# Kernel tuning notes

Hardware: AMD Instinct MI355X
Metric: run time of the kernel (lower is better)

Reference implementation:

```python
import jax, jax.numpy as jnp
import numpy as np

B, NC, NF, D = 4, 256, 768, 768
TOK_RATIO = 0.5
LN_EPS = 1e-5


def _linear(x, w, b):
    # w: [D_in, D_out]
    return x @ w + b


def _leaky(x):
    return jax.nn.leaky_relu(x, negative_slope=0.01)


def setup_inputs() -> dict:
    key = jax.random.key(0)
    ks = jax.random.split(key, 12)
    s = 1.0 / np.sqrt(D)
    inp = {
        "cls_tokens": jax.random.normal(ks[0], (B, NC, D), dtype=jnp.float32),
        "feats": jax.random.normal(ks[1], (B, NF, D), dtype=jnp.float32),
        "W_head_w": jax.random.uniform(ks[2], (D, D), minval=-s, maxval=s),
        "W_head_b": jax.random.uniform(ks[3], (D,), minval=-s, maxval=s),
        "W_tail_w": jax.random.uniform(ks[4], (D, D), minval=-s, maxval=s),
        "W_tail_b": jax.random.uniform(ks[5], (D,), minval=-s, maxval=s),
        "lin1_w": jax.random.uniform(ks[6], (D, D), minval=-s, maxval=s),
        "lin1_b": jax.random.uniform(ks[7], (D,), minval=-s, maxval=s),
        "lin2_w": jax.random.uniform(ks[8], (D, D), minval=-s, maxval=s),
        "lin2_b": jax.random.uniform(ks[9], (D,), minval=-s, maxval=s),
        "ln_w": jnp.ones((D,), dtype=jnp.float32),
        "ln_b": jnp.zeros((D,), dtype=jnp.float32),
    }
    return inp


def reference(cls_tokens, feats, W_head_w, W_head_b, W_tail_w, W_tail_b,
              lin1_w, lin1_b, lin2_w, lin2_b, ln_w, ln_b):
    topk = int(TOK_RATIO * NC)
    scale = D ** (-0.5)

    # feats is detached in the original (clone().detach())
    x = jnp.concatenate([cls_tokens, jax.lax.stop_gradient(feats)], axis=1)  # [B, Nt, D]

    e_h = _linear(cls_tokens, W_head_w, W_head_b)  # [B, Nc, D]
    e_t = _linear(x, W_tail_w, W_tail_b)           # [B, Nt, D]

    attn_logit = jnp.einsum('bnd,bmd->bnm', e_h * scale, e_t)  # [B, Nc, Nt]
    topk_weight, topk_index = jax.lax.top_k(attn_logit, topk)  # [B, Nc, k]

    # Gather neighbor embeddings: Nb_h[b, n, j] = e_t[b, topk_index[b, n, j]]
    Nb_h = jax.vmap(lambda et, idx: et[idx])(e_t, topk_index)  # [B, Nc, k, D]

    topk_prob = jax.nn.softmax(topk_weight, axis=2)            # [B, Nc, k]
    p = topk_prob[..., None]
    eh_r = p * Nb_h + (1.0 - p) * e_h[:, :, None, :]           # [B, Nc, k, D]

    gate = jnp.tanh(e_h[:, :, None, :] + eh_r)
    ka_weight = jnp.einsum('bnkd,bnkd->bnk', Nb_h, gate)
    ka_prob = jax.nn.softmax(ka_weight, axis=2)
    e_Nh = jnp.einsum('bnk,bnkd->bnd', ka_prob, Nb_h)          # [B, Nc, D]

    # bi-interaction aggregation
    sum_emb = _leaky(_linear((e_h + e_Nh) * 0.1 + cls_tokens, lin1_w, lin1_b))
    bi_emb = _leaky(_linear(e_h * e_Nh * 0.1 + cls_tokens, lin2_w, lin2_b))
    embedding = sum_emb + bi_emb

    # LayerNorm (dropout is a no-op: p=0 and output overwritten in original)
    mu = jnp.mean(embedding, axis=-1, keepdims=True)
    var = jnp.var(embedding, axis=-1, keepdims=True)
    h = (embedding - mu) * jax.lax.rsqrt(var + LN_EPS) * ln_w + ln_b
    return h
```

## Files before the change

### kernel.cpp

```cpp
#include <hip/hip_runtime.h>
#include <hip/hip_bf16.h>
#include <math.h>

#define DDIM 768
#define NCLS 256
#define NFEAT 768
#define NTOK 1024
#define NBATCH 4
#define KSEL 128

typedef float f32x4 __attribute__((ext_vector_type(4)));
typedef float f32x2 __attribute__((ext_vector_type(2)));
typedef short s16x8 __attribute__((ext_vector_type(8)));

#if __has_builtin(__builtin_amdgcn_exp2f)
#define EXP2F __builtin_amdgcn_exp2f
#else
#define EXP2F(x) __expf(0.6931471805599453f * (x))
#endif

__device__ __forceinline__ float wsum(float v) {
#pragma unroll
  for (int o = 32; o; o >>= 1) v += __shfl_down(v, o, 64);
  return v;
}
__device__ __forceinline__ float wmaxr(float v) {
#pragma unroll
  for (int o = 32; o; o >>= 1) v = fmaxf(v, __shfl_down(v, o, 64));
  return v;
}
__device__ __forceinline__ short f2bf(float f) {
  union { __hip_bfloat16 h; short s; } u;
  u.h = __float2bfloat16(f);
  return u.s;
}
__device__ __forceinline__ float bf2f(short s) {
  union { unsigned u; float f; } c;
  c.u = ((unsigned)(unsigned short)s) << 16;
  return c.f;
}
__device__ __forceinline__ f32x2 bfpair(unsigned w) {
  f32x2 r;
  r.x = __uint_as_float(w << 16);
  r.y = __uint_as_float(w & 0xffff0000u);
  return r;
}
__device__ __forceinline__ void cvt8(float4 x, float4 y, s16x8& h, s16x8& l) {
  float v[8] = {x.x, x.y, x.z, x.w, y.x, y.y, y.z, y.w};
#pragma unroll
  for (int i = 0; i < 8; ++i) {
    short hh = f2bf(v[i]);
    h[i] = hh;
    l[i] = f2bf(v[i] - bf2f(hh));
  }
}
__device__ __forceinline__ int swz(int row, int chunk) {
  return (row << 5) + (((chunk ^ (row >> 1)) & 3) << 3);
}

__global__ __launch_bounds__(256) void prep_all(
    const float* __restrict__ cls, const float* __restrict__ feats,
    const float* __restrict__ w0, const float* __restrict__ w1,
    const float* __restrict__ w2, const float* __restrict__ w3,
    short* __restrict__ h0, short* __restrict__ h1, short* __restrict__ h2,
    short* __restrict__ h3, short* __restrict__ l0, short* __restrict__ l1,
    short* __restrict__ Xh, short* __restrict__ Xl) {
  __shared__ float tile[32][33];
  const int bid = blockIdx.x;
  const int t = threadIdx.x;
  if (bid < 2304) {
    const int z = bid / 576, rem = bid % 576;
    const int by = rem / 24, bx = rem % 24;
    const float* s = z == 0 ? w0 : z == 1 ? w1 : z == 2 ? w2 : w3;
    short* dh = z == 0 ? h0 : z == 1 ? h1 : z == 2 ? h2 : h3;
    short* dl = z == 0 ? l0 : z == 1 ? l1 : nullptr;
    const int tx = t & 31, ty0 = t >> 5;
    const int r0 = by * 32, c0 = bx * 32;
#pragma unroll
    for (int i = 0; i < 4; ++i) {
      int ty = ty0 + i * 8;
      tile[ty][tx] = s[(size_t)(r0 + ty) * DDIM + c0 + tx];
    }
    __syncthreads();
#pragma unroll
    for (int i = 0; i < 4; ++i) {
      int ty = ty0 + i * 8;
      float v = tile[tx][ty];
      short hh = f2bf(v);
      dh[(size_t)(c0 + ty) * DDIM + r0 + tx] = hh;
      if (dl) dl[(size_t)(c0 + ty) * DDIM + r0 + tx] = f2bf(v - bf2f(hh));
    }
  } else {
    const size_t base = ((size_t)(bid - 2304) * 256 + t) * 8;
    const int row = (int)(base / DDIM);
    const int col = (int)(base % DDIM);
    const int b = row >> 10, rr = row & 1023;
    const float* src =
        (rr < NCLS) ? cls + ((size_t)b * NCLS + rr) * DDIM + col
                    : feats + ((size_t)b * NFEAT + (rr - NCLS)) * DDIM + col;
    float4 a0 = *(const float4*)(src);
    float4 a1 = *(const float4*)(src + 4);
    s16x8 h, l;
    cvt8(a0, a1, h, l);
    *(s16x8*)(Xh + base) = h;
    *(s16x8*)(Xl + base) = l;
  }
}

__global__ __launch_bounds__(256) void gemm_front(
    const short* __restrict__ Xh, const short* __restrict__ Xl,
    const short* __restrict__ WhT_h, const short* __restrict__ WhT_l,
    const float* __restrict__ Whb, const short* __restrict__ WtT_h,
    const short* __restrict__ WtT_l, const float* __restrict__ Wtb,
    short* __restrict__ eh_hi, short* __restrict__ eh_lo,
    short* __restrict__ et_hi, short* __restrict__ et_lo) {
  __shared__ short Ah[128 * 32], Al[128 * 32];
  __shared__ short Bh[64 * 32], Bl[64 * 32];
  const int bid = blockIdx.x;
  const int xcd = bid & 7, idx = bid >> 3;
  const int ytile = xcd * 5 + idx / 12;
  const int xtile = idx % 12;
  const int t = threadIdx.x;
  const int row0 = ytile * 128, col0 = xtile * 64;
  const bool head = row0 < 1024;

  const int ar = t >> 1, ac = (t & 1) * 2;
  const int aw0 = swz(ar, ac), aw1 = swz(ar, ac + 1);
  size_t xrow;
  {
    int gr = row0 + ar;
    xrow = head ? (size_t)(((gr >> 8) << 10) + (gr & 255)) : (size_t)(gr - 1024);
  }
  const short* aph = Xh + xrow * DDIM + ac * 8;
  const short* apl = Xl + xrow * DDIM + ac * 8;
  const int br = t >> 2, bc = t & 3;
  const int bw0 = swz(br, bc);
  const short* bph = (head ? WhT_h : WtT_h) + (size_t)(col0 + br) * DDIM + bc * 8;
  const short* bpl = (head ? WhT_l : WtT_l) + (size_t)(col0 + br) * DDIM + bc * 8;
  const float* biasu = head ? Whb : Wtb;

  const int lane = t & 63, wave = t >> 6;
  const int wr = wave >> 1, wc = wave & 1;
  const int fr = lane & 15, fq = lane >> 4;

  f32x4 acc[4][2] = {};
  s16x8 rah0 = *(const s16x8*)(aph);
  s16x8 rah1 = *(const s16x8*)(aph + 8);
  s16x8 ral0 = *(const s16x8*)(apl);
  s16x8 ral1 = *(const s16x8*)(apl + 8);
  s16x8 rbh = *(const s16x8*)(bph);
  s16x8 rbl = *(const s16x8*)(bpl);

  for (int kt = 0; kt < 24; ++kt) {
    __syncthreads();
    *(s16x8*)&Ah[aw0] = rah0;
    *(s16x8*)&Ah[aw1] = rah1;
    *(s16x8*)&Al[aw0] = ral0;
    *(s16x8*)&Al[aw1] = ral1;
    *(s16x8*)&Bh[bw0] = rbh;
    *(s16x8*)&Bl[bw0] = rbl;
    __syncthreads();
    const int kn = (kt < 23 ? kt + 1 : 23) * 32;
    rah0 = *(const s16x8*)(aph + kn);
    rah1 = *(const s16x8*)(aph + kn + 8);
    ral0 = *(const s16x8*)(apl + kn);
    ral1 = *(const s16x8*)(apl + kn + 8);
    rbh = *(const s16x8*)(bph + kn);
    rbl = *(const s16x8*)(bpl + kn);

    s16x8 afh[4], afl[4];
#pragma unroll
    for (int m = 0; m < 4; ++m) {
      int ao = swz(wr * 64 + m * 16 + fr, fq);
      afh[m] = *(const s16x8*)&Ah[ao];
      afl[m] = *(const s16x8*)&Al[ao];
    }
#pragma unroll
    for (int n = 0; n < 2; ++n) {
      int bo = swz(wc * 32 + n * 16 + fr, fq);
      s16x8 bfh = *(const s16x8*)&Bh[bo];
      s16x8 bfl = *(const s16x8*)&Bl[bo];
#pragma unroll
      for (int m = 0; m < 4; ++m) {
        acc[m][n] =
            __builtin_amdgcn_mfma_f32_16x16x32_bf16(afh[m], bfh, acc[m][n], 0, 0, 0);
        acc[m][n] =
            __builtin_amdgcn_mfma_f32_16x16x32_bf16(afh[m], bfl, acc[m][n], 0, 0, 0);
        acc[m][n] =
            __builtin_amdgcn_mfma_f32_16x16x32_bf16(afl[m], bfh, acc[m][n], 0, 0, 0);
      }
    }
  }

  short* Ch = head ? eh_hi : et_hi;
  short* Cl = head ? eh_lo : et_lo;
  const int rbase = head ? row0 : row0 - 1024;
#pragma unroll
  for (int m = 0; m < 4; ++m) {
#pragma unroll
    for (int n = 0; n < 2; ++n) {
#pragma unroll
      for (int r = 0; r < 4; ++r) {
        int rg = rbase + wr * 64 + m * 16 + fq * 4 + r;
        int cg = col0 + wc * 32 + n * 16 + fr;
        float v = acc[m][n][r] + biasu[cg];
        size_t o = (size_t)rg * DDIM + cg;
        short hh = f2bf(v);
        Ch[o] = hh;
        Cl[o] = f2bf(v - bf2f(hh));
      }
    }
  }
}

__global__ __launch_bounds__(256) void gemm_logits(
    const short* __restrict__ eh_hi, const short* __restrict__ eh_lo,
    const short* __restrict__ et_hi, const short* __restrict__ et_lo,
    float* __restrict__ logits, float scale) {
  __shared__ short Ah[32 * 32], Al[32 * 32];
  __shared__ short Bh[64 * 32], Bl[64 * 32];
  const int bid = blockIdx.x;
  const int xcd = bid & 7, idx = bid >> 3;
  const int batch = xcd >> 1;
  const int sub = ((xcd & 1) << 6) | idx;
  const int xtile = sub & 15, ytile = sub >> 4;
  const int row0 = ytile * 32, col0 = xtile * 64;
  const int t = threadIdx.x;

  const int ahalf = t >> 7, ac2 = t & 127;
  const int asr = ac2 >> 2, acc_ = ac2 & 3;
  const short* aptr = (ahalf ? eh_lo : eh_hi) +
                      ((size_t)batch * NCLS + row0 + asr) * DDIM + acc_ * 8;
  const int aso = swz(asr, acc_);
  const int bsr = t >> 2, bcc = t & 3;
  const short* bph = et_hi + ((size_t)batch * NTOK + col0 + bsr) * DDIM + bcc * 8;
  const short* bpl = et_lo + ((size_t)batch * NTOK + col0 + bsr) * DDIM + bcc * 8;
  const int bso = swz(bsr, bcc);

  const int lane = t & 63, wave = t >> 6;
  const int wr = wave >> 1, wc = wave & 1;
  const int fr = lane & 15, fq = lane >> 4;

  f32x4 acc[2] = {};
  s16x8 rA = *(const s16x8*)(aptr);
  s16x8 rbh = *(const s16x8*)(bph);
  s16x8 rbl = *(const s16x8*)(bpl);

  for (int kt = 0; kt < 24; ++kt) {
    __syncthreads();
    *(s16x8*)&(ahalf ? Al : Ah)[aso] = rA;
    *(s16x8*)&Bh[bso] = rbh;
    *(s16x8*)&Bl[bso] = rbl;
    __syncthreads();
    const int kn = (kt < 23 ? kt + 1 : 23) * 32;
    rA = *(const s16x8*)(aptr + kn);
    rbh = *(const s16x8*)(bph + kn);
    rbl = *(const s16x8*)(bpl + kn);
    int ao = swz(wr * 16 + fr, fq);
    s16x8 afh = *(const s16x8*)&Ah[ao];
    s16x8 afl = *(const s16x8*)&Al[ao];
#pragma unroll
    for (int n = 0; n < 2; ++n) {
      int bo = swz(wc * 32 + n * 16 + fr, fq);
      s16x8 bfh = *(const s16x8*)&Bh[bo];
      s16x8 bfl = *(const s16x8*)&Bl[bo];
      acc[n] = __builtin_amdgcn_mfma_f32_16x16x32_bf16(afh, bfh, acc[n], 0, 0, 0);
      acc[n] = __builtin_amdgcn_mfma_f32_16x16x32_bf16(afh, bfl, acc[n], 0, 0, 0);
      acc[n] = __builtin_amdgcn_mfma_f32_16x16x32_bf16(afl, bfh, acc[n], 0, 0, 0);
    }
  }

  float* Cb = logits + (size_t)batch * NCLS * NTOK;
#pragma unroll
  for (int n = 0; n < 2; ++n)
#pragma unroll
    for (int r = 0; r < 4; ++r) {
      int rg = row0 + wr * 16 + fq * 4 + r;
      int cg = col0 + wc * 32 + n * 16 + fr;
      Cb[(size_t)rg * NTOK + cg] = scale * acc[n][r];
    }
}

__global__ __launch_bounds__(512) void select_agg(
    const float* __restrict__ logits, const short* __restrict__ eh_hi,
    const short* __restrict__ et_hi, const float* __restrict__ cls,
    short* __restrict__ inbf) {
  const int bid = blockIdx.x;
  const int xcd = bid & 7, slot = bid >> 3;
  const int batch = xcd >> 1;
  const int row = batch * 256 + (xcd & 1) * 128 + slot;
  const int t = threadIdx.x, lane = t & 63, wave = t >> 6;

  __shared__ int hist[256];
  __shared__ int sh_bin, sh_rem;
  __shared__ int cnt;
  __shared__ int wsumT[8];
  __shared__ float p_sh[KSEL];
  __shared__ int idx_sh[KSEL];
  __shared__ float kaw_sh[KSEL];
  __shared__ float red[2];

  float2 v2 = *(const float2*)(logits + (size_t)row * NTOK + 2 * t);
  float val[2] = {v2.x, v2.y};
  unsigned key[2];
#pragma unroll
  for (int i = 0; i < 2; ++i) {
    unsigned u = __float_as_uint(val[i]);
    key[i] = (u & 0x80000000u) ? ~u : (u | 0x80000000u);
  }
  unsigned pref = 0, mask = 0;
  int rem = KSEL;
#pragma unroll
  for (int shift = 24; shift >= 0; shift -= 8) {
    if (t < 256) hist[t] = 0;
    __syncthreads();
#pragma unroll
    for (int i = 0; i < 2; ++i)
      if ((key[i] & mask) == pref)
        atomicAdd(&hist[(key[i] >> shift) & 255], 1);
    __syncthreads();
    if (wave == 0) {
      int h0 = hist[4 * lane], h1 = hist[4 * lane + 1];
      int h2 = hist[4 * lane + 2], h3 = hist[4 * lane + 3];
      int s = h0 + h1 + h2 + h3;
#pragma unroll
      for (int o = 1; o < 64; o <<= 1) {
        int v = __shfl_down(s, o, 64);
        if (lane + o < 64) s += v;
      }
      int abv = __shfl_down(s, 1, 64);
      if (lane == 63) abv = 0;
      int c3 = abv + h3, c2 = c3 + h2, c1 = c2 + h1, c0 = c1 + h0;
      int bin = -1, nab = 0;
      if (c3 >= rem && abv < rem) { bin = 4 * lane + 3; nab = abv; }
      else if (c2 >= rem && c3 < rem) { bin = 4 * lane + 2; nab = c3; }
      else if (c1 >= rem && c2 < rem) { bin = 4 * lane + 1; nab = c2; }
      else if (c0 >= rem && c1 < rem) { bin = 4 * lane + 0; nab = c1; }
      if (bin >= 0) { sh_bin = bin; sh_rem = rem - nab; }
    }
    __syncthreads();
    pref |= ((unsigned)sh_bin) << shift;
    mask |= 0xFFu << shift;
    rem = sh_rem;
  }
  const unsigned T = pref;
  const int above = KSEL - rem;

  if (t == 0) cnt = 0;
  int tc = (key[0] == T) + (key[1] == T);
  int inc = tc;
#pragma unroll
  for (int o = 1; o < 64; o <<= 1) {
    int v = __shfl_up(inc, o, 64);
    if (lane >= o) inc += v;
  }
  if (lane == 63) wsumT[wave] = inc;
  __syncthreads();
  int wbase = 0;
#pragma unroll
  for (int w = 0; w < 8; ++w)
    if (w < wave) wbase += wsumT[w];
  int excl = wbase + inc - tc;
#pragma unroll
  for (int i = 0; i < 2; ++i) {
    if (key[i] > T) {
      int s2 = atomicAdd(&cnt, 1);
      p_sh[s2] = val[i];
      idx_sh[s2] = 2 * t + i;
    } else if (key[i] == T) {
      int r = excl++;
      if (r < rem) {
        p_sh[above + r] = val[i];
        idx_sh[above + r] = 2 * t + i;
      }
    }
  }
  __syncthreads();

  if (wave == 0) {
    float m = wmaxr(fmaxf(p_sh[lane], p_sh[lane + 64]));
    if (!lane) red[0] = m;
  }
  __syncthreads();
  if (t < KSEL) p_sh[t] = __expf(p_sh[t] - red[0]);
  __syncthreads();
  if (wave == 0) {
    float s = wsum(p_sh[lane] + p_sh[lane + 64]);
    if (!lane) red[1] = s;
  }
  __syncthreads();
  if (t < KSEL) p_sh[t] *= (1.f / red[1]);
  __syncthreads();

  f32x2 eh2[6];
  {
    const short* ehrow = eh_hi + (size_t)row * DDIM;
    s16x8 e8 = *(const s16x8*)(ehrow + 8 * lane);
    short4 e4 = *(const short4*)(ehrow + 512 + 4 * lane);
    const unsigned* w8 = (const unsigned*)&e8;
    const unsigned* w4 = (const unsigned*)&e4;
#pragma unroll
    for (int i = 0; i < 4; ++i) eh2[i] = bfpair(w8[i]);
    eh2[4] = bfpair(w4[0]);
    eh2[5] = bfpair(w4[1]);
  }
  const short* etb = et_hi + (size_t)batch * NTOK * DDIM;
  const float LOG2E = 1.4426950408889634f;

  {
    const int jb = wave * 16;
    const short* nb0 = etb + (size_t)idx_sh[jb] * DDIM;
    s16x8 n8 = *(const s16x8*)(nb0 + 8 * lane);
    short4 n4 = *(const short4*)(nb0 + 512 + 4 * lane);
    for (int i = 0; i < 16; ++i) {
      const int j = jb + i;
      s16x8 n8n;
      short4 n4n;
      if (i < 15) {
        const short* nbn = etb + (size_t)idx_sh[j + 1] * DDIM;
        n8n = *(const s16x8*)(nbn + 8 * lane);
        n4n = *(const short4*)(nbn + 512 + 4 * lane);
      }
      float pj = p_sh[j];
      float a2 = (4.f - 2.f * pj) * LOG2E;
      float b22 = (2.f * pj) * LOG2E;
      f32x2 av = {a2, a2}, bv = {b22, b22};
      f32x2 acc2 = {0.f, 0.f};
      const unsigned* w8 = (const unsigned*)&n8;
      const unsigned* w4 = (const unsigned*)&n4;
      f32x2 nq2[6];
#pragma unroll
      for (int q = 0; q < 4; ++q) nq2[q] = bfpair(w8[q]);
      nq2[4] = bfpair(w4[0]);
      nq2[5] = bfpair(w4[1]);
#pragma unroll
      for (int q = 0; q < 6; ++q) {
        f32x2 arg = av * eh2[q] + bv * nq2[q];
        f32x2 ex;
        ex.x = EXP2F(arg.x);
        ex.y = EXP2F(arg.y);
        f32x2 den = ex + (f32x2){1.f, 1.f};
        f32x2 r;
        r.x = __builtin_amdgcn_rcpf(den.x);
        r.y = __builtin_amdgcn_rcpf(den.y);
        f32x2 g = r * (f32x2){-2.f, -2.f} + (f32x2){1.f, 1.f};
        acc2 = nq2[q] * g + acc2;
      }
      float partial = acc2.x + acc2.y;
      partial = wsum(partial);
      if (!lane) kaw_sh[j] = partial;
      n8 = n8n;
      n4 = n4n;
    }
  }
  __syncthreads();

  if (wave == 0) {
    float m = wmaxr(fmaxf(kaw_sh[lane], kaw_sh[lane + 64]));
    if (!lane) red[0] = m;
  }
  __syncthreads();
  if (t < KSEL) kaw_sh[t] = __expf(kaw_sh[t] - red[0]);
  __syncthreads();
  if (wave == 0) {
    float s = wsum(kaw_sh[lane] + kaw_sh[lane + 64]);
    if (!lane) red[1] = s;
  }
  __syncthreads();
  if (t < KSEL) kaw_sh[t] *= (1.f / red[1]);
  __syncthreads();

  if (t < 384) {
    const size_t o = (size_t)row * DDIM + 2 * t;
    unsigned ehw = *(const unsigned*)(eh_hi + o);
    f32x2 eh = bfpair(ehw);
    float2 cl2 = *(const float2*)(cls + o);
    f32x2 cl = {cl2.x, cl2.y};
    f32x2 acc = {0.f, 0.f};
#pragma unroll 8
    for (int j = 0; j < KSEL; ++j) {
      float pr = kaw_sh[j];
      unsigned w = *(const unsigned*)(etb + (size_t)idx_sh[j] * DDIM + 2 * t);
      f32x2 nb = bfpair(w);
      acc = nb * (f32x2){pr, pr} + acc;
    }
    f32x2 sv = (eh + acc) * (f32x2){0.1f, 0.1f} + cl;
    f32x2 bvv = (eh * acc) * (f32x2){0.1f, 0.1f} + cl;
    short2 s2, b2;
    s2.x = f2bf(sv.x);
    s2.y = f2bf(sv.y);
    b2.x = f2bf(bvv.x);
    b2.y = f2bf(bvv.y);
    *(short2*)&inbf[o] = s2;
    *(short2*)&inbf[(size_t)(NBATCH * NCLS) * DDIM + o] = b2;
  }
}

__global__ __launch_bounds__(256) void gemm_lin(
    const short* __restrict__ inbf, const short* __restrict__ L1T,
    const short* __restrict__ L2T, const float* __restrict__ b1,
    const float* __restrict__ b2, float* __restrict__ emb) {
  __shared__ short A1[32 * 32], A2[32 * 32];
  __shared__ short B1[64 * 32], B2[64 * 32];
  const int bid = blockIdx.x;
  const int xcd = bid & 7, idx = bid >> 3;
  const int ytile = xcd * 4 + idx / 12, xtile = idx % 12;
  const int t = threadIdx.x;
  const int row0 = ytile * 32, col0 = xtile * 64;

  const int ahalf = t >> 7, at = t & 127;
  const int asr = at >> 2, asc = at & 3;
  const short* aptr = inbf + (ahalf ? (size_t)1024 * DDIM : 0) +
                      (size_t)(row0 + asr) * DDIM + asc * 8;
  const int aso = swz(asr, asc);
  const int bsr = t >> 2, bsc = t & 3;
  const short* b1p = L1T + (size_t)(col0 + bsr) * DDIM + bsc * 8;
  const short* b2p = L2T + (size_t)(col0 + bsr) * DDIM + bsc * 8;
  const int bso = swz(bsr, bsc);

  const int lane = t & 63, wave = t >> 6;
  const int wr = wave >> 1, wc = wave & 1;
  const int fr = lane & 15, fq = lane >> 4;

  f32x4 acc1[2] = {}, acc2[2] = {};
  s16x8 rA = *(const s16x8*)(aptr);
  s16x8 rB1 = *(const s16x8*)(b1p);
  s16x8 rB2 = *(const s16x8*)(b2p);
  for (int kt = 0; kt < 24; ++kt) {
    __syncthreads();
    *(s16x8*)&(ahalf ? A2 : A1)[aso] = rA;
    *(s16x8*)&B1[bso] = rB1;
    *(s16x8*)&B2[bso] = rB2;
    __syncthreads();
    const int kn = (kt < 23 ? kt + 1 : 23) * 32;
    rA = *(const s16x8*)(aptr + kn);
    rB1 = *(const s16x8*)(b1p + kn);
    rB2 = *(const s16x8*)(b2p + kn);
    int ao = swz(wr * 16 + fr, fq);
    s16x8 a1f = *(const s16x8*)&A1[ao];
    s16x8 a2f = *(const s16x8*)&A2[ao];
#pragma unroll
    for (int n = 0; n < 2; ++n) {
      int bo = swz(wc * 32 + n * 16 + fr, fq);
      s16x8 b1f = *(const s16x8*)&B1[bo];
      s16x8 b2f = *(const s16x8*)&B2[bo];
      acc1[n] = __builtin_amdgcn_mfma_f32_16x16x32_bf16(a1f, b1f, acc1[n], 0, 0, 0);
      acc2[n] = __builtin_amdgcn_mfma_f32_16x16x32_bf16(a2f, b2f, acc2[n], 0, 0, 0);
    }
  }
#pragma unroll
  for (int n = 0; n < 2; ++n)
#pragma unroll
    for (int r = 0; r < 4; ++r) {
      int rg = row0 + wr * 16 + fq * 4 + r;
      int cg = col0 + wc * 32 + n * 16 + fr;
      float v1 = acc1[n][r] + b1[cg];
      v1 = v1 > 0.f ? v1 : 0.01f * v1;
      float v2 = acc2[n][r] + b2[cg];
      v2 = v2 > 0.f ? v2 : 0.01f * v2;
      emb[(size_t)rg * DDIM + cg] = v1 + v2;
    }
}

__global__ __launch_bounds__(256) void ln_kernel(const float* __restrict__ emb,
                                                 const float* __restrict__ lw,
                                                 const float* __restrict__ lb,
                                                 float* __restrict__ out) {
  const int row = blockIdx.x;
  const int t = threadIdx.x;
  const int lane = t & 63, wave = t >> 6;
  __shared__ float red[4];
  __shared__ float bs[2];
  float e[3];
#pragma unroll
  for (int c = 0; c < 3; ++c) e[c] = emb[(size_t)row * DDIM + t + 256 * c];
  float s = e[0] + e[1] + e[2];
  s = wsum(s);
  if (lane == 0) red[wave] = s;
  __syncthreads();
  if (t == 0) bs[0] = (red[0] + red[1] + red[2] + red[3]) * (1.f / DDIM);
  __syncthreads();
  float mu = bs[0];
  float q = 0.f;
#pragma unroll
  for (int c = 0; c < 3; ++c) {
    float d = e[c] - mu;
    q = fmaf(d, d, q);
  }
  q = wsum(q);
  if (lane == 0) red[wave] = q;
  __syncthreads();
  if (t == 0) bs[1] = (red[0] + red[1] + red[2] + red[3]) * (1.f / DDIM);
  __syncthreads();
  float rstd = rsqrtf(bs[1] + 1e-5f);
#pragma unroll
  for (int c = 0; c < 3; ++c) {
    int d = t + 256 * c;
    out[(size_t)row * DDIM + d] = (e[c] - mu) * rstd * lw[d] + lb[d];
  }
}

extern "C" void kernel_launch(void* const* d_in, const int* in_sizes, int n_in,
                              void* d_out, int out_size, void* d_ws,
                              size_t ws_size, hipStream_t stream) {
  const float* cls = (const float*)d_in[0];
  const float* feats = (const float*)d_in[1];
  const float* Whw = (const float*)d_in[2];
  const float* Whb = (const float*)d_in[3];
  const float* Wtw = (const float*)d_in[4];
  const float* Wtb = (const float*)d_in[5];
  const float* l1w = (const float*)d_in[6];
  const float* l1b = (const float*)d_in[7];
  const float* l2w = (const float*)d_in[8];
  const float* l2b = (const float*)d_in[9];
  const float* lnw = (const float*)d_in[10];
  const float* lnb = (const float*)d_in[11];
  float* out = (float*)d_out;

  float* ws = (float*)d_ws;
  float* emb = ws;
  short* eh_hi = (short*)(ws + 3932160);
  short* eh_lo = eh_hi + 786432;
  short* et_hi = (short*)(ws + 4718592);
  short* et_lo = et_hi + 3145728;
  short* WhT_h = (short*)(ws + 7864320);
  short* WhT_l = WhT_h + 589824;
  short* WtT_h = WhT_h + 2 * 589824;
  short* WtT_l = WhT_h + 3 * 589824;
  short* L1T = (short*)(ws + 9043968);
  short* L2T = L1T + 589824;
  float* logits = ws + 7864320;
  short* Xh = (short*)(ws + 9633792);
  short* Xl = Xh + 3145728;
  short* inbf = (short*)(ws + 10027008);
  (void)ws_size;
  (void)in_sizes;
  (void)n_in;
  (void)out_size;

  const float scale = 0.036084391824351615f;
  dim3 blk(256);

  prep_all<<<dim3(3840), blk, 0, stream>>>(cls, feats, Whw, Wtw, l1w, l2w,
                                           WhT_h, WtT_h, L1T, L2T, WhT_l,
                                           WtT_l, Xh, Xl);
  gemm_front<<<dim3(480), blk, 0, stream>>>(
      Xh, Xl, WhT_h, WhT_l, Whb, WtT_h, WtT_l, Wtb, eh_hi, eh_lo, et_hi,
      et_lo);
  gemm_logits<<<dim3(512), blk, 0, stream>>>(eh_hi, eh_lo, et_hi, et_lo,
                                             logits, scale);
  select_agg<<<dim3(1024), dim3(512), 0, stream>>>(logits, eh_hi, et_hi, cls,
                                                   inbf);
  gemm_lin<<<dim3(384), blk, 0, stream>>>(inbf, L1T, L2T, l1b, l2b, emb);
  ln_kernel<<<dim3(NBATCH * NCLS), blk, 0, stream>>>(emb, lnw, lnb, out);
}
```

Measured before the change: 110.9 us.

## Split top-k selection from aggregation and privatize radix histograms per wave

The fused select_agg kernel is split into two kernels. topk_sm runs the radix top-k and softmax and writes probabilities and indices to a workspace buffer. agg_sm reloads them and performs the gated neighbor aggregation. The radix histogram becomes per-wave (8x256) to cut shared-memory atomic contention, and wave 0 sums the eight copies. The trade is an extra kernel launch, a global round-trip for the top-k results, and more histogram clearing work per pass, in exchange for lower atomic contention and the ability to tune each phase on its own.

```diff
diff --git a/kernel.cpp b/kernel.cpp
--- a/kernel.cpp
+++ b/kernel.cpp
@@ -281,23 +281,21 @@
     }
 }
 
-__global__ __launch_bounds__(512) void select_agg(
-    const float* __restrict__ logits, const short* __restrict__ eh_hi,
-    const short* __restrict__ et_hi, const float* __restrict__ cls,
-    short* __restrict__ inbf) {
+__global__ __launch_bounds__(512) void topk_sm(const float* __restrict__ logits,
+                                               float* __restrict__ pbuf,
+                                               int* __restrict__ ibuf) {
   const int bid = blockIdx.x;
   const int xcd = bid & 7, slot = bid >> 3;
   const int batch = xcd >> 1;
   const int row = batch * 256 + (xcd & 1) * 128 + slot;
   const int t = threadIdx.x, lane = t & 63, wave = t >> 6;
 
-  __shared__ int hist[256];
+  __shared__ int hist[8][256];
   __shared__ int sh_bin, sh_rem;
   __shared__ int cnt;
   __shared__ int wsumT[8];
   __shared__ float p_sh[KSEL];
   __shared__ int idx_sh[KSEL];
-  __shared__ float kaw_sh[KSEL];
   __shared__ float red[2];
 
   float2 v2 = *(const float2*)(logits + (size_t)row * NTOK + 2 * t);
@@ -312,16 +310,26 @@
   int rem = KSEL;
 #pragma unroll
   for (int shift = 24; shift >= 0; shift -= 8) {
-    if (t < 256) hist[t] = 0;
+    int* hflat = &hist[0][0];
+    hflat[t] = 0;
+    hflat[t + 512] = 0;
+    hflat[t + 1024] = 0;
+    hflat[t + 1536] = 0;
     __syncthreads();
 #pragma unroll
     for (int i = 0; i < 2; ++i)
       if ((key[i] & mask) == pref)
-        atomicAdd(&hist[(key[i] >> shift) & 255], 1);
+        atomicAdd(&hist[wave][(key[i] >> shift) & 255], 1);
     __syncthreads();
     if (wave == 0) {
-      int h0 = hist[4 * lane], h1 = hist[4 * lane + 1];
-      int h2 = hist[4 * lane + 2], h3 = hist[4 * lane + 3];
+      int h0 = 0, h1 = 0, h2 = 0, h3 = 0;
+#pragma unroll
+      for (int w = 0; w < 8; ++w) {
+        h0 += hist[w][4 * lane];
+        h1 += hist[w][4 * lane + 1];
+        h2 += hist[w][4 * lane + 2];
+        h3 += hist[w][4 * lane + 3];
+      }
       int s = h0 + h1 + h2 + h3;
 #pragma unroll
       for (int o = 1; o < 64; o <<= 1) {
@@ -389,7 +397,31 @@
     if (!lane) red[1] = s;
   }
   __syncthreads();
-  if (t < KSEL) p_sh[t] *= (1.f / red[1]);
+  if (t < KSEL) {
+    pbuf[(size_t)row * KSEL + t] = p_sh[t] * (1.f / red[1]);
+    ibuf[(size_t)row * KSEL + t] = idx_sh[t];
+  }
+}
+
+__global__ __launch_bounds__(512) void agg_sm(
+    const float* __restrict__ pbuf, const int* __restrict__ ibuf,
+    const short* __restrict__ eh_hi, const short* __restrict__ et_hi,
+    const float* __restrict__ cls, short* __restrict__ inbf) {
+  const int bid = blockIdx.x;
+  const int xcd = bid & 7, slot = bid >> 3;
+  const int batch = xcd >> 1;
+  const int row = batch * 256 + (xcd & 1) * 128 + slot;
+  const int t = threadIdx.x, lane = t & 63, wave = t >> 6;
+
+  __shared__ float p_sh[KSEL];
+  __shared__ int idx_sh[KSEL];
+  __shared__ float kaw_sh[KSEL];
+  __shared__ float red[2];
+
+  if (t < KSEL) {
+    p_sh[t] = pbuf[(size_t)row * KSEL + t];
+    idx_sh[t] = ibuf[(size_t)row * KSEL + t];
+  }
   __syncthreads();
 
   f32x2 eh2[6];
@@ -443,8 +475,8 @@
         f32x2 r;
         r.x = __builtin_amdgcn_rcpf(den.x);
         r.y = __builtin_amdgcn_rcpf(den.y);
-        f32x2 g = r * (f32x2){-2.f, -2.f} + (f32x2){1.f, 1.f};
-        acc2 = nq2[q] * g + acc2;
+        f32x2 gg = r * (f32x2){-2.f, -2.f} + (f32x2){1.f, 1.f};
+        acc2 = nq2[q] * gg + acc2;
       }
       float partial = acc2.x + acc2.y;
       partial = wsum(partial);
@@ -633,6 +665,8 @@
   short* Xh = (short*)(ws + 9633792);
   short* Xl = Xh + 3145728;
   short* inbf = (short*)(ws + 10027008);
+  float* pbuf = ws + 10813440;
+  int* ibuf = (int*)(ws + 10944512);
   (void)ws_size;
   (void)in_sizes;
   (void)n_in;
@@ -649,8 +683,9 @@
       et_lo);
   gemm_logits<<<dim3(512), blk, 0, stream>>>(eh_hi, eh_lo, et_hi, et_lo,
                                              logits, scale);
-  select_agg<<<dim3(1024), dim3(512), 0, stream>>>(logits, eh_hi, et_hi, cls,
-                                                   inbf);
+  topk_sm<<<dim3(1024), dim3(512), 0, stream>>>(logits, pbuf, ibuf);
+  agg_sm<<<dim3(1024), dim3(512), 0, stream>>>(pbuf, ibuf, eh_hi, et_hi, cls,
+                                               inbf);
   gemm_lin<<<dim3(384), blk, 0, stream>>>(inbf, L1T, L2T, l1b, l2b, emb);
   ln_kernel<<<dim3(NBATCH * NCLS), blk, 0, stream>>>(emb, lnw, lnb, out);
 }
```

After: 114.6 us. 3.3% more time.

## Fuse ka-softmax and weighted neighbor sum via online softmax in gate loop

Applied to the files above, without the earlier changes.

Replaces the separate softmax over ka weights and the second pass that re-gathers all 128 neighbor rows from global memory with an online-softmax accumulation inside the gate loop, reusing the neighbor values already in registers. Each wave keeps a running max, sum and a rescaled weighted sum; the waves are then merged through shared memory with a cross-wave max/sum rescale. This removes a full second gather of neighbor embeddings and several block barriers, at the cost of extra registers, a data-dependent rescale branch, and about 26KB more shared memory, which could reduce occupancy.

```diff
diff --git a/kernel.cpp b/kernel.cpp
--- a/kernel.cpp
+++ b/kernel.cpp
@@ -297,8 +297,9 @@
   __shared__ int wsumT[8];
   __shared__ float p_sh[KSEL];
   __shared__ int idx_sh[KSEL];
-  __shared__ float kaw_sh[KSEL];
   __shared__ float red[2];
+  __shared__ float mw_sh[8], sw_sh[8];
+  __shared__ float pE_sh[8 * 64 * 13];
 
   float2 v2 = *(const float2*)(logits + (size_t)row * NTOK + 2 * t);
   float val[2] = {v2.x, v2.y};
@@ -407,6 +408,9 @@
   const short* etb = et_hi + (size_t)batch * NTOK * DDIM;
   const float LOG2E = 1.4426950408889634f;
 
+  float m_w = -3.0e38f, s_w = 0.f;
+  f32x2 pE0 = {0.f, 0.f}, pE1 = {0.f, 0.f}, pE2 = {0.f, 0.f};
+  f32x2 pE3 = {0.f, 0.f}, pE4 = {0.f, 0.f}, pE5 = {0.f, 0.f};
   {
     const int jb = wave * 16;
     const short* nb0 = etb + (size_t)idx_sh[jb] * DDIM;
@@ -446,44 +450,78 @@
         f32x2 g = r * (f32x2){-2.f, -2.f} + (f32x2){1.f, 1.f};
         acc2 = nq2[q] * g + acc2;
       }
-      float partial = acc2.x + acc2.y;
-      partial = wsum(partial);
-      if (!lane) kaw_sh[j] = partial;
+      float kaw = acc2.x + acc2.y;
+#pragma unroll
+      for (int o = 32; o; o >>= 1) kaw += __shfl_xor(kaw, o, 64);
+      if (kaw > m_w) {
+        float f = EXP2F((m_w - kaw) * LOG2E);
+        f32x2 fv = {f, f};
+        s_w *= f;
+        pE0 *= fv; pE1 *= fv; pE2 *= fv;
+        pE3 *= fv; pE4 *= fv; pE5 *= fv;
+        m_w = kaw;
+      }
+      float c = EXP2F((kaw - m_w) * LOG2E);
+      s_w += c;
+      f32x2 cc = {c, c};
+      pE0 = nq2[0] * cc + pE0;
+      pE1 = nq2[1] * cc + pE1;
+      pE2 = nq2[2] * cc + pE2;
+      pE3 = nq2[3] * cc + pE3;
+      pE4 = nq2[4] * cc + pE4;
+      pE5 = nq2[5] * cc + pE5;
       n8 = n8n;
       n4 = n4n;
     }
   }
-  __syncthreads();
-
-  if (wave == 0) {
-    float m = wmaxr(fmaxf(kaw_sh[lane], kaw_sh[lane + 64]));
-    if (!lane) red[0] = m;
-  }
-  __syncthreads();
-  if (t < KSEL) kaw_sh[t] = __expf(kaw_sh[t] - red[0]);
-  __syncthreads();
-  if (wave == 0) {
-    float s = wsum(kaw_sh[lane] + kaw_sh[lane + 64]);
-    if (!lane) red[1] = s;
-  }
-  __syncthreads();
-  if (t < KSEL) kaw_sh[t] *= (1.f / red[1]);
+  if (!lane) {
+    mw_sh[wave] = m_w;
+    sw_sh[wave] = s_w;
+  }
+  __syncthreads();
+
+  float gm = mw_sh[0];
+#pragma unroll
+  for (int w = 1; w < 8; ++w) gm = fmaxf(gm, mw_sh[w]);
+  float denom = 0.f;
+#pragma unroll
+  for (int w = 0; w < 8; ++w) denom += sw_sh[w] * EXP2F((mw_sh[w] - gm) * LOG2E);
+  {
+    float fw = EXP2F((m_w - gm) * LOG2E);
+    f32x2 fv = {fw, fw};
+    float* base = &pE_sh[(wave * 64 + lane) * 13];
+    f32x2 t0 = pE0 * fv, t1 = pE1 * fv, t2 = pE2 * fv;
+    f32x2 t3 = pE3 * fv, t4 = pE4 * fv, t5 = pE5 * fv;
+    base[0] = t0.x;  base[1] = t0.y;  base[2] = t1.x;  base[3] = t1.y;
+    base[4] = t2.x;  base[5] = t2.y;  base[6] = t3.x;  base[7] = t3.y;
+    base[8] = t4.x;  base[9] = t4.y;  base[10] = t5.x; base[11] = t5.y;
+  }
   __syncthreads();
 
   if (t < 384) {
-    const size_t o = (size_t)row * DDIM + 2 * t;
+    const int d0 = 2 * t;
+    int l0, s0;
+    if (d0 < 512) {
+      l0 = d0 >> 3;
+      s0 = d0 & 7;
+    } else {
+      l0 = (d0 - 512) >> 2;
+      s0 = 8 + ((d0 - 512) & 3);
+    }
+    float sum0 = 0.f, sum1 = 0.f;
+#pragma unroll
+    for (int w = 0; w < 8; ++w) {
+      const float* b = &pE_sh[(w * 64 + l0) * 13 + s0];
+      sum0 += b[0];
+      sum1 += b[1];
+    }
+    float inv = 1.f / denom;
+    f32x2 acc = {sum0 * inv, sum1 * inv};
+    const size_t o = (size_t)row * DDIM + d0;
     unsigned ehw = *(const unsigned*)(eh_hi + o);
     f32x2 eh = bfpair(ehw);
     float2 cl2 = *(const float2*)(cls + o);
     f32x2 cl = {cl2.x, cl2.y};
-    f32x2 acc = {0.f, 0.f};
-#pragma unroll 8
-    for (int j = 0; j < KSEL; ++j) {
-      float pr = kaw_sh[j];
-      unsigned w = *(const unsigned*)(etb + (size_t)idx_sh[j] * DDIM + 2 * t);
-      f32x2 nb = bfpair(w);
-      acc = nb * (f32x2){pr, pr} + acc;
-    }
     f32x2 sv = (eh + acc) * (f32x2){0.1f, 0.1f} + cl;
     f32x2 bvv = (eh * acc) * (f32x2){0.1f, 0.1f} + cl;
     short2 s2, b2;
```

Result: faster. 108.5 us, median of 2 (-2.2%).
